# Performance work log

Hardware: AMD Instinct MI355X
Metric: run time of the kernel (lower is better)

The kernel has to match this reference:

```python
import jax, jax.numpy as jnp
import numpy as np

N_HEADS = 16


def layernorm(x, g, b, eps=1e-5):
    mu = jnp.mean(x, axis=-1, keepdims=True)
    var = jnp.var(x, axis=-1, keepdims=True)
    return (x - mu) * jax.lax.rsqrt(var + eps) * g + b


def mha(x, w_qkv, b_qkv, w_o, b_o, n_heads):
    # standard multi-head self-attention (dropout off / eval mode)
    B, S, D = x.shape
    hd = D // n_heads
    qkv = x @ w_qkv + b_qkv                      # [B,S,3D]
    q, k, v = jnp.split(qkv, 3, axis=-1)
    q = q.reshape(B, S, n_heads, hd).transpose(0, 2, 1, 3)  # bhsd
    k = k.reshape(B, S, n_heads, hd).transpose(0, 2, 1, 3)
    v = v.reshape(B, S, n_heads, hd).transpose(0, 2, 1, 3)
    att = jnp.einsum('bhqd,bhkd->bhqk', q, k) / jnp.sqrt(jnp.asarray(hd, x.dtype))
    att = jax.nn.softmax(att, axis=-1)
    out = jnp.einsum('bhqk,bhkd->bhqd', att, v)
    out = out.transpose(0, 2, 1, 3).reshape(B, S, D)
    return out @ w_o + b_o


def setup_inputs() -> dict:
    key = jax.random.key(0)
    ks = jax.random.split(key, 12)
    B, Sx, Sz, D = 4, 1024, 1024, 1024
    H = D * 4
    s = 0.02
    return {
        'x': jax.random.normal(ks[0], (B, Sx, D), jnp.float32),
        'z': jax.random.normal(ks[1], (B, Sz, D), jnp.float32),
        'g1': jnp.ones((D,), jnp.float32),
        'b1': jnp.zeros((D,), jnp.float32),
        'w_qkv': jax.random.normal(ks[2], (D, 3 * D), jnp.float32) * s,
        'b_qkv': jnp.zeros((3 * D,), jnp.float32),
        'w_o': jax.random.normal(ks[3], (D, D), jnp.float32) * s,
        'b_o': jnp.zeros((D,), jnp.float32),
        'w_kv': jax.random.normal(ks[4], (D, 2 * D), jnp.float32) * s,
        'b_kv': jnp.zeros((2 * D,), jnp.float32),
        'g2': jnp.ones((D,), jnp.float32),
        'b2': jnp.zeros((D,), jnp.float32),
        'w_m1': jax.random.normal(ks[5], (D, H), jnp.float32) * s,
        'b_m1': jnp.zeros((H,), jnp.float32),
        'w_m2': jax.random.normal(ks[6], (H, D), jnp.float32) * s,
        'b_m2': jnp.zeros((D,), jnp.float32),
    }


def reference(x, z, g1, b1, w_qkv, b_qkv, w_o, b_o, w_kv, b_kv, g2, b2, w_m1, b_m1, w_m2, b_m2):
    # q = x + self_mha(ln1(x))
    q = x + mha(layernorm(x, g1, b1), w_qkv, b_qkv, w_o, b_o, N_HEADS)
    # single-head cross attention: k,v from z, scale by sqrt(dim)
    kv = z @ w_kv + b_kv
    k, v = jnp.split(kv, 2, axis=-1)            # each [B,Sz,D]
    scale = jnp.sqrt(jnp.asarray(k.shape[-1], x.dtype))
    att = jax.nn.softmax(jnp.einsum('bqd,bkd->bqk', q, k) / scale, axis=-1)
    out = jnp.einsum('bqk,bkd->bqd', att, v)
    # out = out + mlp(ln2(out))
    h = layernorm(out, g2, b2)
    h = jax.nn.gelu(h @ w_m1 + b_m1) @ w_m2 + b_m2
    return out + h
```

## Files before the change

kernel.cpp:

```cpp
#include <hip/hip_runtime.h>
#include <cstdint>
#include <cstddef>

using u16 = unsigned short;

typedef __attribute__((ext_vector_type(4))) float f32x4;
typedef __attribute__((ext_vector_type(8))) short bf16x8;

#define DEV static __device__ __forceinline__

DEV float bf2f(u16 v) {
  union { unsigned u; float f; } x; x.u = ((unsigned)v) << 16; return x.f;
}
DEV u16 f2bf(float f) {
  union { float f; unsigned u; } x; x.f = f;
  unsigned r = x.u + 0x7fffu + ((x.u >> 16) & 1u);
  return (u16)(r >> 16);
}
DEV void gload16(const void* g, void* l) {
  __builtin_amdgcn_global_load_lds((const __attribute__((address_space(1))) void*)g,
                                   (__attribute__((address_space(3))) void*)l, 16, 0, 0);
}
DEV float fast_gelu(float x) {
  const float y = 0.7978845608028654f * (x + 0.044715f * x * x * x);
  const float e = __builtin_amdgcn_exp2f(y * 2.8853900817779268f);
  const float t = 1.0f - 2.0f * __builtin_amdgcn_rcpf(e + 1.0f);
  return 0.5f * x * (1.0f + t);
}

DEV float rowmax16_dpp(float v) {
  union { float f; int i; } a, b;
  a.f = v;
  b.i = __builtin_amdgcn_update_dpp(0, a.i, 0x121, 0xf, 0xf, true); a.f = fmaxf(a.f, b.f);
  b.i = __builtin_amdgcn_update_dpp(0, a.i, 0x122, 0xf, 0xf, true); a.f = fmaxf(a.f, b.f);
  b.i = __builtin_amdgcn_update_dpp(0, a.i, 0x124, 0xf, 0xf, true); a.f = fmaxf(a.f, b.f);
  b.i = __builtin_amdgcn_update_dpp(0, a.i, 0x128, 0xf, 0xf, true); a.f = fmaxf(a.f, b.f);
  return a.f;
}

template <typename OutT, bool GELU, int BN, bool SPLIT>
DEV void gemm_body(
    const u16* __restrict__ A, const u16* __restrict__ Bt, OutT* __restrict__ C,
    int K, int lda, int ldb, int ldc,
    const float* __restrict__ bias,
    const float* __restrict__ resF, const u16* __restrict__ resB, int ldr,
    float scale, long long sA, long long sB, long long sC, long long sR,
    int kSlices, int bx, int by, int z,
    u16* As , u16* Bs )
{
  constexpr int NW = (BN == 128) ? 64 : 32;
  constexpr int NJ = NW / 16;
  constexpr int BH = BN * 32;

  const int bz = z / kSlices;
  const int ks = z - bz * kSlices;
  const int Ksl = K / kSlices;
  const int kbeg = ks * Ksl, kend = kbeg + Ksl;

  A  += (size_t)bz * sA;
  Bt += (size_t)bz * sB;
  if constexpr (SPLIT) C += (size_t)ks * sC;
  else                 C += (size_t)bz * sC;
  const int m0 = by * 128, n0 = bx * BN;
  const int tid = threadIdx.x;
  const int lane = tid & 63, wave = tid >> 6;
  const int wm = (wave >> 1) * 64, wn = (wave & 1) * NW;
  const int m15 = lane & 15, quad = lane >> 4;

  const u16* Ab = A + (size_t)m0 * lda;
  const u16* Bb = Bt + (size_t)n0 * ldb;
  const int r0 = tid >> 2, cc8 = (tid & 3) * 8;

  f32x4 acc[4][NJ];
#pragma unroll
  for (int i = 0; i < 4; i++)
#pragma unroll
    for (int j = 0; j < NJ; j++) acc[i][j] = (f32x4){0.f, 0.f, 0.f, 0.f};

  for (int k0 = kbeg; k0 < kend; k0 += 64) {
    __syncthreads();
#pragma unroll
    for (int h = 0; h < 2; h++) {
      const int kc = k0 + h * 32 + cc8;
      u16* Ah = As + h * 4096;
      gload16(Ab + (size_t)r0 * lda + kc,        Ah + tid * 8);
      gload16(Ab + (size_t)(r0 + 64) * lda + kc, Ah + 2048 + tid * 8);
      u16* Bh = Bs + h * BH;
      gload16(Bb + (size_t)r0 * ldb + kc,        Bh + tid * 8);
      if constexpr (BN == 128)
        gload16(Bb + (size_t)(r0 + 64) * ldb + kc, Bh + 2048 + tid * 8);
    }
    __syncthreads();
#pragma unroll
    for (int h = 0; h < 2; h++) {
      bf16x8 af[4], bfr[NJ];
#pragma unroll
      for (int i = 0; i < 4; i++)
        af[i] = *(const bf16x8*)&As[h * 4096 + (wm + i * 16 + m15) * 32 + quad * 8];
#pragma unroll
      for (int j = 0; j < NJ; j++)
        bfr[j] = *(const bf16x8*)&Bs[h * BH + (wn + j * 16 + m15) * 32 + quad * 8];
#pragma unroll
      for (int i = 0; i < 4; i++)
#pragma unroll
        for (int j = 0; j < NJ; j++)
          acc[i][j] = __builtin_amdgcn_mfma_f32_16x16x32_bf16(af[i], bfr[j], acc[i][j], 0, 0, 0);
    }
  }

  const float* resFb = resF ? resF + (size_t)bz * sR : nullptr;
  const u16*   resBb = resB ? resB + (size_t)bz * sR : nullptr;

#pragma unroll
  for (int i = 0; i < 4; i++) {
    const int rowb = m0 + wm + i * 16 + quad * 4;
#pragma unroll
    for (int r = 0; r < 4; r++) {
      const size_t rowoff = (size_t)(rowb + r) * ldc;
      const size_t resoff = (size_t)(rowb + r) * ldr;
#pragma unroll
      for (int j = 0; j < NJ; j++) {
        const int col = n0 + wn + j * 16 + m15;
        float v = acc[i][j][r] * scale;
        if constexpr (SPLIT) {
          ((u16*)C)[rowoff + col] = f2bf(v);
        } else {
          if (bias) v += bias[col];
          if (GELU) v = fast_gelu(v);
          if (resFb) v += resFb[resoff + col];
          if (resBb) v += bf2f(resBb[resoff + col]);
          if constexpr (sizeof(OutT) == 4) C[rowoff + col] = v;
          else ((u16*)C)[rowoff + col] = f2bf(v);
        }
      }
    }
  }
}

template <typename OutT, bool GELU, int BN, bool SPLIT>
__global__ __launch_bounds__(256, 4) void gemm_nt(
    const u16* __restrict__ A, const u16* __restrict__ Bt, OutT* __restrict__ C,
    int K, int lda, int ldb, int ldc,
    const float* __restrict__ bias,
    const float* __restrict__ resF, const u16* __restrict__ resB, int ldr,
    float scale, long long sA, long long sB, long long sC, long long sR,
    int kSlices)
{
  __shared__ u16 As[128 * 64];
  __shared__ u16 Bs[BN * 64];
  gemm_body<OutT, GELU, BN, SPLIT>(A, Bt, C, K, lda, ldb, ldc, bias, resF, resB,
                                   ldr, scale, sA, sB, sC, sR, kSlices,
                                   blockIdx.x, blockIdx.y, blockIdx.z, As, Bs);
}

__global__ __launch_bounds__(256, 4) void gemm_dual(
    const u16* __restrict__ A1, const u16* __restrict__ B1, u16* __restrict__ C1,
    int ldc1, const float* __restrict__ bias1, int nx1,
    const u16* __restrict__ A2, const u16* __restrict__ B2, u16* __restrict__ C2,
    int ldc2, const float* __restrict__ bias2)
{
  __shared__ u16 As[128 * 64];
  __shared__ u16 Bs[128 * 64];
  const int bx = blockIdx.x;
  if (bx < nx1)
    gemm_body<u16, false, 128, false>(A1, B1, C1, 1024, 1024, 1024, ldc1, bias1,
                                      nullptr, nullptr, 0, 1.0f, 0, 0, 0, 0, 1,
                                      bx, blockIdx.y, 0, As, Bs);
  else
    gemm_body<u16, false, 128, false>(A2, B2, C2, 1024, 1024, 1024, ldc2, bias2,
                                      nullptr, nullptr, 0, 1.0f, 0, 0, 0, 0, 1,
                                      bx - nx1, blockIdx.y, 0, As, Bs);
}

__global__ __launch_bounds__(256) void mlp2_reduce_k(
    const u16* __restrict__ part, long long sliceStride,
    const u16* __restrict__ outb, const float* __restrict__ b_m2,
    float* __restrict__ outF)
{
  const size_t i = (size_t)blockIdx.x * 256 + threadIdx.x;
  const int col = (int)((i * 4) & 1023);
  const ushort4 u = ((const ushort4*)outb)[i];
  float4 o;
  o.x = bf2f(u.x) + b_m2[col + 0];
  o.y = bf2f(u.y) + b_m2[col + 1];
  o.z = bf2f(u.z) + b_m2[col + 2];
  o.w = bf2f(u.w) + b_m2[col + 3];
#pragma unroll
  for (int ks = 0; ks < 4; ks++) {
    const ushort4 p = ((const ushort4*)(part + (size_t)ks * sliceStride))[i];
    o.x += bf2f(p.x); o.y += bf2f(p.y); o.z += bf2f(p.z); o.w += bf2f(p.w);
  }
  ((float4*)outF)[i] = o;
}

__global__ __launch_bounds__(256) void prep_all_k(
    const float* __restrict__ w_qkv, const float* __restrict__ w_o,
    const float* __restrict__ w_kv,  const float* __restrict__ w_m1,
    const float* __restrict__ w_m2,
    u16* __restrict__ wqkvT, u16* __restrict__ woT, u16* __restrict__ wkvT,
    u16* __restrict__ wm1T,  u16* __restrict__ wm2T,
    const float* __restrict__ x, const float* __restrict__ g1,
    const float* __restrict__ b1, u16* __restrict__ xln,
    const float* __restrict__ z, u16* __restrict__ zb)
{
  __shared__ u16 tile[32][33];
  __shared__ float red[8];
  int idx = blockIdx.x;
  const int t = threadIdx.x;
  if (idx >= 14336) {
    idx -= 14336;
    if (idx >= 4096) {
      const size_t i = (size_t)(idx - 4096) * 256 + t;
      const float4 f = ((const float4*)z)[i];
      ushort4 o; o.x = f2bf(f.x); o.y = f2bf(f.y); o.z = f2bf(f.z); o.w = f2bf(f.w);
      ((ushort4*)zb)[i] = o;
      return;
    }
    const int row = idx;
    float v[4];
    const float4 f = ((const float4*)(x + (size_t)row * 1024))[t];
    v[0] = f.x; v[1] = f.y; v[2] = f.z; v[3] = f.w;
    float s = v[0] + v[1] + v[2] + v[3];
    float sq = v[0]*v[0] + v[1]*v[1] + v[2]*v[2] + v[3]*v[3];
#pragma unroll
    for (int off = 1; off < 64; off <<= 1) { s += __shfl_xor(s, off); sq += __shfl_xor(sq, off); }
    const int wv = t >> 6;
    if ((t & 63) == 0) { red[wv] = s; red[4 + wv] = sq; }
    __syncthreads();
    s = red[0] + red[1] + red[2] + red[3];
    sq = red[4] + red[5] + red[6] + red[7];
    const float mean = s * (1.0f / 1024.0f);
    const float var = sq * (1.0f / 1024.0f) - mean * mean;
    const float rstd = rsqrtf(var + 1e-5f);
    const int c = t * 4;
    ushort4 o;
    o.x = f2bf((v[0] - mean) * rstd * g1[c + 0] + b1[c + 0]);
    o.y = f2bf((v[1] - mean) * rstd * g1[c + 1] + b1[c + 1]);
    o.z = f2bf((v[2] - mean) * rstd * g1[c + 2] + b1[c + 2]);
    o.w = f2bf((v[3] - mean) * rstd * g1[c + 3] + b1[c + 3]);
    ((ushort4*)(xln + (size_t)row * 1024))[t] = o;
    return;
  }
  const float* in; u16* out; int gx, ldin, ldout;
  if (idx < 3072)      { in = w_qkv; out = wqkvT; gx = 96;  ldin = 3072; ldout = 1024; }
  else if (idx < 4096) { idx -= 3072; in = w_o;  out = woT;  gx = 32;  ldin = 1024; ldout = 1024; }
  else if (idx < 6144) { idx -= 4096; in = w_kv; out = wkvT; gx = 64;  ldin = 2048; ldout = 1024; }
  else if (idx < 10240){ idx -= 6144; in = w_m1; out = wm1T; gx = 128; ldin = 4096; ldout = 1024; }
  else                 { idx -= 10240; in = w_m2; out = wm2T; gx = 32; ldin = 1024; ldout = 4096; }
  const int bx = idx % gx, by = idx / gx;
  const int tx = t & 31, ty = t >> 5;
  const int xx = bx * 32 + tx;
#pragma unroll
  for (int j = 0; j < 4; j++)
    tile[ty + j * 8][tx] = f2bf(in[(size_t)(by * 32 + ty + j * 8) * ldin + xx]);
  __syncthreads();
  const int x2 = by * 32 + tx;
#pragma unroll
  for (int j = 0; j < 4; j++)
    out[(size_t)(bx * 32 + ty + j * 8) * ldout + x2] = tile[tx][ty + j * 8];
}

__global__ __launch_bounds__(256) void transpose_v_self(
    const u16* __restrict__ qkv, u16* __restrict__ vT)
{
  __shared__ u16 tile[32][33];
  const int z = blockIdx.z, b = z >> 4, h = z & 15;
  const u16* in = qkv + (size_t)b * 1024 * 3072 + 2048 + h * 64;
  u16* out = vT + (size_t)z * 64 * 1024;
  const int tx = threadIdx.x & 31, ty = threadIdx.x >> 5;
  const int key0 = blockIdx.x * 32, d0 = blockIdx.y * 32;
#pragma unroll
  for (int j = 0; j < 4; j++)
    tile[ty + j * 8][tx] = in[(size_t)(key0 + ty + j * 8) * 3072 + d0 + tx];
  __syncthreads();
#pragma unroll
  for (int j = 0; j < 4; j++)
    out[(size_t)(d0 + ty + j * 8) * 1024 + key0 + tx] = tile[tx][ty + j * 8];
}

__global__ __launch_bounds__(256, 5) void flash_self_attn3(
    const u16* __restrict__ qkv, const u16* __restrict__ vT, u16* __restrict__ outp)
{
  __shared__ u16 Ks[64 * 72];
  __shared__ u16 Vs[64 * 72];
  __shared__ u16 Ps[4][16 * 72];
  const int b = blockIdx.z, h = blockIdx.y, q0 = blockIdx.x * 64;
  const int tid = threadIdx.x;
  const int lane = tid & 63, w = tid >> 6;
  const int m15 = lane & 15, quad = lane >> 4;
  const float L2E = 1.4426950408889634f;

  const size_t base = (size_t)b * 1024 * 3072;
  const u16* qb  = qkv + base + (size_t)q0 * 3072 + h * 64;
  const u16* kb  = qkv + base + 1024 + h * 64;
  const u16* vtb = vT + (size_t)(b * 16 + h) * 64 * 1024;

  const int r8 = tid >> 3, c8 = (tid & 7) * 8;

  bf16x8 aq[2];
#pragma unroll
  for (int kk = 0; kk < 2; kk++) {
    const bf16x8 raw = *(const bf16x8*)(qb + (size_t)(w * 16 + m15) * 3072 + kk * 32 + quad * 8);
#pragma unroll
    for (int j = 0; j < 8; j++)
      ((u16*)&aq[kk])[j] = f2bf(bf2f(((const u16*)&raw)[j]) * 0.125f);
  }

  const short oneb = (short)0x3F80;
  const bf16x8 ones = {oneb, oneb, oneb, oneb, oneb, oneb, oneb, oneb};

  float mL[4];
  f32x4 lacc;
  f32x4 oacc[4];
#pragma unroll
  for (int r = 0; r < 4; r++) mL[r] = -3.0e38f;
  lacc = (f32x4){0.f, 0.f, 0.f, 0.f};
#pragma unroll
  for (int d = 0; d < 4; d++) oacc[d] = (f32x4){0.f, 0.f, 0.f, 0.f};

  for (int kt = 0; kt < 16; kt++) {
    const int key0 = kt * 64;
    bf16x8 kreg[2], vreg[2];
#pragma unroll
    for (int i = 0; i < 2; i++) {
      kreg[i] = *(const bf16x8*)(kb + (size_t)(key0 + r8 + i * 32) * 3072 + c8);
      vreg[i] = *(const bf16x8*)(vtb + (size_t)(r8 + i * 32) * 1024 + key0 + c8);
    }
    __syncthreads();
#pragma unroll
    for (int i = 0; i < 2; i++) {
      *(bf16x8*)&Ks[(r8 + i * 32) * 72 + c8] = kreg[i];
      *(bf16x8*)&Vs[(r8 + i * 32) * 72 + c8] = vreg[i];
    }
    __syncthreads();

    f32x4 sacc[4];
#pragma unroll
    for (int n = 0; n < 4; n++) sacc[n] = (f32x4){0.f, 0.f, 0.f, 0.f};
#pragma unroll
    for (int kk = 0; kk < 2; kk++)
#pragma unroll
      for (int n = 0; n < 4; n++) {
        const bf16x8 bk = *(const bf16x8*)&Ks[(n * 16 + m15) * 72 + kk * 32 + quad * 8];
        sacc[n] = __builtin_amdgcn_mfma_f32_16x16x32_bf16(aq[kk], bk, sacc[n], 0, 0, 0);
      }

    float al[4];
#pragma unroll
    for (int r = 0; r < 4; r++) {
      float v = fmaxf(fmaxf(sacc[0][r], sacc[1][r]), fmaxf(sacc[2][r], sacc[3][r]));
      v = rowmax16_dpp(v) * L2E;
      const float mnew = fmaxf(mL[r], v);
      al[r] = __builtin_amdgcn_exp2f(mL[r] - mnew);
      mL[r] = mnew;
    }
#pragma unroll
    for (int n = 0; n < 4; n++)
#pragma unroll
      for (int r = 0; r < 4; r++) {
        const float p = __builtin_amdgcn_exp2f(fmaf(sacc[n][r], L2E, -mL[r]));
        Ps[w][(quad * 4 + r) * 72 + n * 16 + m15] = f2bf(p);
      }
#pragma unroll
    for (int r = 0; r < 4; r++) {
      lacc[r] *= al[r];
#pragma unroll
      for (int d = 0; d < 4; d++) oacc[d][r] *= al[r];
    }

    bf16x8 ap[2];
    ap[0] = *(const bf16x8*)&Ps[w][m15 * 72 + quad * 8];
    ap[1] = *(const bf16x8*)&Ps[w][m15 * 72 + 32 + quad * 8];
    lacc = __builtin_amdgcn_mfma_f32_16x16x32_bf16(ap[0], ones, lacc, 0, 0, 0);
    lacc = __builtin_amdgcn_mfma_f32_16x16x32_bf16(ap[1], ones, lacc, 0, 0, 0);
#pragma unroll
    for (int kk = 0; kk < 2; kk++)
#pragma unroll
      for (int d = 0; d < 4; d++) {
        const bf16x8 bv = *(const bf16x8*)&Vs[(d * 16 + m15) * 72 + kk * 32 + quad * 8];
        oacc[d] = __builtin_amdgcn_mfma_f32_16x16x32_bf16(ap[kk], bv, oacc[d], 0, 0, 0);
      }
  }

  u16* ob = outp + (size_t)(b * 1024 + q0 + w * 16 + quad * 4) * 1024 + h * 64 + m15;
#pragma unroll
  for (int r = 0; r < 4; r++) {
    const float inv = 1.0f / lacc[r];
#pragma unroll
    for (int d = 0; d < 4; d++)
      ob[(size_t)r * 1024 + d * 16] = f2bf(oacc[d][r] * inv);
  }
}

__global__ __launch_bounds__(256) void layernorm_b_k(
    const u16* __restrict__ x, const float* __restrict__ g, const float* __restrict__ bb,
    u16* __restrict__ y)
{
  const int row = blockIdx.x;
  const int t = threadIdx.x;
  float v[4];
  const ushort4 u = ((const ushort4*)(x + (size_t)row * 1024))[t];
  v[0] = bf2f(u.x); v[1] = bf2f(u.y); v[2] = bf2f(u.z); v[3] = bf2f(u.w);
  float s = v[0] + v[1] + v[2] + v[3];
  float sq = v[0]*v[0] + v[1]*v[1] + v[2]*v[2] + v[3]*v[3];
#pragma unroll
  for (int off = 1; off < 64; off <<= 1) { s += __shfl_xor(s, off); sq += __shfl_xor(sq, off); }
  __shared__ float red[8];
  const int wv = t >> 6;
  if ((t & 63) == 0) { red[wv] = s; red[4 + wv] = sq; }
  __syncthreads();
  s = red[0] + red[1] + red[2] + red[3];
  sq = red[4] + red[5] + red[6] + red[7];
  const float mean = s * (1.0f / 1024.0f);
  const float var = sq * (1.0f / 1024.0f) - mean * mean;
  const float rstd = rsqrtf(var + 1e-5f);
  const int c = t * 4;
  ushort4 o;
  o.x = f2bf((v[0] - mean) * rstd * g[c + 0] + bb[c + 0]);
  o.y = f2bf((v[1] - mean) * rstd * g[c + 1] + bb[c + 1]);
  o.z = f2bf((v[2] - mean) * rstd * g[c + 2] + bb[c + 2]);
  o.w = f2bf((v[3] - mean) * rstd * g[c + 3] + bb[c + 3]);
  ((ushort4*)(y + (size_t)row * 1024))[t] = o;
}

__global__ __launch_bounds__(256) void softmax_vt_k(
    const float* __restrict__ S, u16* __restrict__ P,
    const u16* __restrict__ kv, u16* __restrict__ vT)
{
  __shared__ u16 tile[32][33];
  __shared__ float red[8];
  const int t = threadIdx.x;
  int idx = blockIdx.x;
  if (idx >= 4096) {
    idx -= 4096;
    const int bx = idx & 31, by = (idx >> 5) & 31, bz = idx >> 10;
    const u16* in = kv + 1024 + (size_t)bz * 2097152;
    u16* out = vT + (size_t)bz * 1048576;
    const int tx = t & 31, ty = t >> 5;
    const int x = bx * 32 + tx;
#pragma unroll
    for (int j = 0; j < 4; j++)
      tile[ty + j * 8][tx] = in[(size_t)(by * 32 + ty + j * 8) * 2048 + x];
    __syncthreads();
    const int x2 = by * 32 + tx;
#pragma unroll
    for (int j = 0; j < 4; j++)
      out[(size_t)(bx * 32 + ty + j * 8) * 1024 + x2] = tile[tx][ty + j * 8];
    return;
  }
  const int row = idx;
  const float4 f = ((const float4*)(S + (size_t)row * 1024))[t];
  float mx = fmaxf(fmaxf(f.x, f.y), fmaxf(f.z, f.w));
#pragma unroll
  for (int off = 1; off < 64; off <<= 1) mx = fmaxf(mx, __shfl_xor(mx, off));
  const int wv = t >> 6;
  if ((t & 63) == 0) red[wv] = mx;
  __syncthreads();
  mx = fmaxf(fmaxf(red[0], red[1]), fmaxf(red[2], red[3]));
  float e0 = __expf(f.x - mx), e1 = __expf(f.y - mx), e2 = __expf(f.z - mx), e3 = __expf(f.w - mx);
  float s = e0 + e1 + e2 + e3;
#pragma unroll
  for (int off = 1; off < 64; off <<= 1) s += __shfl_xor(s, off);
  if ((t & 63) == 0) red[4 + wv] = s;
  __syncthreads();
  s = red[4] + red[5] + red[6] + red[7];
  const float inv = 1.0f / s;
  ushort4 o; o.x = f2bf(e0 * inv); o.y = f2bf(e1 * inv); o.z = f2bf(e2 * inv); o.w = f2bf(e3 * inv);
  ((ushort4*)(P + (size_t)row * 1024))[t] = o;
}

extern "C" void kernel_launch(void* const* d_in, const int* in_sizes, int n_in,
                              void* d_out, int out_size, void* d_ws, size_t ws_size,
                              hipStream_t stream)
{
  const float* x     = (const float*)d_in[0];
  const float* z     = (const float*)d_in[1];
  const float* g1    = (const float*)d_in[2];
  const float* b1    = (const float*)d_in[3];
  const float* w_qkv = (const float*)d_in[4];
  const float* b_qkv = (const float*)d_in[5];
  const float* w_o   = (const float*)d_in[6];
  const float* b_o   = (const float*)d_in[7];
  const float* w_kv  = (const float*)d_in[8];
  const float* b_kv  = (const float*)d_in[9];
  const float* g2    = (const float*)d_in[10];
  const float* b2    = (const float*)d_in[11];
  const float* w_m1  = (const float*)d_in[12];
  const float* b_m1  = (const float*)d_in[13];
  const float* w_m2  = (const float*)d_in[14];
  const float* b_m2  = (const float*)d_in[15];
  float* outF = (float*)d_out;

  char* ws = (char*)d_ws;
  const size_t MB = 1024ull * 1024ull;
  u16*   qkv   = (u16*)(ws + 0);
  u16*   Pm    = (u16*)(ws + 0);
  u16*   hm    = (u16*)(ws + 0);
  u16*   zb    = (u16*)(ws + 24 * MB);
  u16*   vTs   = (u16*)(ws + 24 * MB);
  u16*   xln   = (u16*)(ws + 32 * MB);
  u16*   mpart = (u16*)(ws + 32 * MB);
  u16*   qbuf  = (u16*)(ws + 40 * MB);
  u16*   kv    = (u16*)(ws + 48 * MB);
  float* Ssc   = (float*)(ws + 64 * MB);
  u16*   h1    = (u16*)(ws + 64 * MB);
  u16*   outb  = (u16*)(ws + 80 * MB);
  u16*   wqkvT = (u16*)(ws + 88 * MB);
  u16*   woT   = (u16*)(ws + 94 * MB);
  u16*   wkvT  = (u16*)(ws + 96 * MB);
  u16*   wm1T  = (u16*)(ws + 100 * MB);
  u16*   wm2T  = (u16*)(ws + 108 * MB);
  u16*   vT    = (u16*)(ws + 116 * MB);

  dim3 blk(256);
  const long long M1 = 1024 * 1024;

  hipLaunchKernelGGL(prep_all_k, dim3(22528), blk, 0, stream,
                     w_qkv, w_o, w_kv, w_m1, w_m2, wqkvT, woT, wkvT, wm1T, wm2T,
                     x, g1, b1, xln, z, zb);
  hipLaunchKernelGGL(gemm_dual, dim3(40, 32, 1), blk, 0, stream,
                     xln, wqkvT, qkv, 3072, b_qkv, 24,
                     zb, wkvT, kv, 2048, b_kv);
  hipLaunchKernelGGL(transpose_v_self, dim3(32, 2, 64), blk, 0, stream, qkv, vTs);
  hipLaunchKernelGGL(flash_self_attn3, dim3(16, 16, 4), blk, 0, stream, qkv, vTs, xln);
  hipLaunchKernelGGL((gemm_nt<u16, false, 64, false>), dim3(16, 32, 1), blk, 0, stream,
                     xln, woT, qbuf, 1024, 1024, 1024, 1024,
                     b_o, x, (const u16*)nullptr, 1024, 1.0f, 0LL, 0LL, 0LL, 0LL, 1);
  hipLaunchKernelGGL((gemm_nt<float, false, 64, false>), dim3(16, 8, 4), blk, 0, stream,
                     qbuf, kv, Ssc, 1024, 1024, 2048, 1024,
                     (const float*)nullptr, (const float*)nullptr, (const u16*)nullptr, 0,
                     0.03125f, M1, 2 * M1, M1, 0LL, 1);
  hipLaunchKernelGGL(softmax_vt_k, dim3(8192), blk, 0, stream, Ssc, Pm, kv, vT);
  hipLaunchKernelGGL((gemm_nt<u16, false, 64, false>), dim3(16, 8, 4), blk, 0, stream,
                     Pm, vT, outb, 1024, 1024, 1024, 1024,
                     (const float*)nullptr, (const float*)nullptr, (const u16*)nullptr, 0,
                     1.0f, M1, M1, M1, 0LL, 1);
  hipLaunchKernelGGL(layernorm_b_k, dim3(4096), blk, 0, stream, (const u16*)outb, g2, b2, h1);
  hipLaunchKernelGGL((gemm_nt<u16, true, 128, false>), dim3(32, 32, 1), blk, 0, stream,
                     h1, wm1T, hm, 1024, 1024, 1024, 4096,
                     b_m1, (const float*)nullptr, (const u16*)nullptr, 0, 1.0f, 0LL, 0LL, 0LL, 0LL, 1);
  hipLaunchKernelGGL((gemm_nt<u16, false, 128, true>), dim3(8, 32, 4), blk, 0, stream,
                     hm, wm2T, mpart, 4096, 4096, 4096, 1024,
                     (const float*)nullptr, (const float*)nullptr, (const u16*)nullptr, 0,
                     1.0f, 0LL, 0LL, 4LL * M1, 0LL, 4);
  hipLaunchKernelGGL(mlp2_reduce_k, dim3(4096), blk, 0, stream,
                     mpart, 4LL * M1, outb, b_m2, outF);
}
```

Measured before the change: 463.9 us.

## Double-buffer GEMM shared-memory tiles to overlap global loads with MFMA compute

Result: slower. 489.3 us (+5.5%).

```diff
diff --git a/kernel.cpp b/kernel.cpp
--- a/kernel.cpp
+++ b/kernel.cpp
@@ -55,7 +55,8 @@
   const int bz = z / kSlices;
   const int ks = z - bz * kSlices;
   const int Ksl = K / kSlices;
-  const int kbeg = ks * Ksl, kend = kbeg + Ksl;
+  const int kbeg = ks * Ksl;
+  const int nIter = Ksl / 32;
 
   A  += (size_t)bz * sA;
   Bt += (size_t)bz * sB;
@@ -77,35 +78,36 @@
 #pragma unroll
     for (int j = 0; j < NJ; j++) acc[i][j] = (f32x4){0.f, 0.f, 0.f, 0.f};
 
-  for (int k0 = kbeg; k0 < kend; k0 += 64) {
-    __syncthreads();
-#pragma unroll
-    for (int h = 0; h < 2; h++) {
-      const int kc = k0 + h * 32 + cc8;
-      u16* Ah = As + h * 4096;
-      gload16(Ab + (size_t)r0 * lda + kc,        Ah + tid * 8);
-      gload16(Ab + (size_t)(r0 + 64) * lda + kc, Ah + 2048 + tid * 8);
-      u16* Bh = Bs + h * BH;
-      gload16(Bb + (size_t)r0 * ldb + kc,        Bh + tid * 8);
-      if constexpr (BN == 128)
-        gload16(Bb + (size_t)(r0 + 64) * ldb + kc, Bh + 2048 + tid * 8);
-    }
-    __syncthreads();
-#pragma unroll
-    for (int h = 0; h < 2; h++) {
-      bf16x8 af[4], bfr[NJ];
-#pragma unroll
-      for (int i = 0; i < 4; i++)
-        af[i] = *(const bf16x8*)&As[h * 4096 + (wm + i * 16 + m15) * 32 + quad * 8];
+  auto issue = [&](int k0, int p) {
+    const int kc = k0 + cc8;
+    u16* Ah = As + p * 4096;
+    gload16(Ab + (size_t)r0 * lda + kc,        Ah + tid * 8);
+    gload16(Ab + (size_t)(r0 + 64) * lda + kc, Ah + 2048 + tid * 8);
+    u16* Bh = Bs + p * BH;
+    gload16(Bb + (size_t)r0 * ldb + kc,        Bh + tid * 8);
+    if constexpr (BN == 128)
+      gload16(Bb + (size_t)(r0 + 64) * ldb + kc, Bh + 2048 + tid * 8);
+  };
+
+  issue(kbeg, 0);
+  __syncthreads();
+  int p = 0;
+  for (int it = 0; it < nIter; ++it) {
+    if (it + 1 < nIter) issue(kbeg + (it + 1) * 32, p ^ 1);
+    bf16x8 af[4], bfr[NJ];
+#pragma unroll
+    for (int i = 0; i < 4; i++)
+      af[i] = *(const bf16x8*)&As[p * 4096 + (wm + i * 16 + m15) * 32 + quad * 8];
+#pragma unroll
+    for (int j = 0; j < NJ; j++)
+      bfr[j] = *(const bf16x8*)&Bs[p * BH + (wn + j * 16 + m15) * 32 + quad * 8];
+#pragma unroll
+    for (int i = 0; i < 4; i++)
 #pragma unroll
       for (int j = 0; j < NJ; j++)
-        bfr[j] = *(const bf16x8*)&Bs[h * BH + (wn + j * 16 + m15) * 32 + quad * 8];
-#pragma unroll
-      for (int i = 0; i < 4; i++)
-#pragma unroll
-        for (int j = 0; j < NJ; j++)
-          acc[i][j] = __builtin_amdgcn_mfma_f32_16x16x32_bf16(af[i], bfr[j], acc[i][j], 0, 0, 0);
-    }
+        acc[i][j] = __builtin_amdgcn_mfma_f32_16x16x32_bf16(af[i], bfr[j], acc[i][j], 0, 0, 0);
+    if (it + 1 < nIter) __syncthreads();
+    p ^= 1;
   }
 
   const float* resFb = resF ? resF + (size_t)bz * sR : nullptr;
@@ -146,8 +148,8 @@
     float scale, long long sA, long long sB, long long sC, long long sR,
     int kSlices)
 {
-  __shared__ u16 As[128 * 64];
-  __shared__ u16 Bs[BN * 64];
+  __shared__ u16 As[2 * 128 * 32];
+  __shared__ u16 Bs[2 * BN * 32];
   gemm_body<OutT, GELU, BN, SPLIT>(A, Bt, C, K, lda, ldb, ldc, bias, resF, resB,
                                    ldr, scale, sA, sB, sC, sR, kSlices,
                                    blockIdx.x, blockIdx.y, blockIdx.z, As, Bs);
@@ -159,8 +161,8 @@
     const u16* __restrict__ A2, const u16* __restrict__ B2, u16* __restrict__ C2,
     int ldc2, const float* __restrict__ bias2)
 {
-  __shared__ u16 As[128 * 64];
-  __shared__ u16 Bs[128 * 64];
+  __shared__ u16 As[2 * 128 * 32];
+  __shared__ u16 Bs[2 * 128 * 32];
   const int bx = blockIdx.x;
   if (bx < nx1)
     gemm_body<u16, false, 128, false>(A1, B1, C1, 1024, 1024, 1024, ldc1, bias1,
```
